# Performance work log

Measured on AMD Instinct MI355X. Metric: run time of the kernel, lower is better.

Reference implementation:

```python
import jax, jax.numpy as jnp
import numpy as np

H, DH, DM = 8, 128, 1024          # n_head, d_head, d_model (n_head*d_head == d_model)
SLEN, BSZ = 256, 64               # slen <= 256 forced by pi0[:, :l]
SCALE = 1.0 / DH ** 0.5
LN_EPS = 1e-5


def setup_inputs() -> dict:
    key = jax.random.key(0)
    k0, k1, k2, k3 = jax.random.split(key, 4)
    h = jax.random.normal(k0, (SLEN, BSZ, DM), jnp.float32)
    W_qkv = jax.random.normal(k1, (H * 4 * DH, DM), jnp.float32) * (DM ** -0.5)
    W_o = jax.random.normal(k2, (DM, H * DH), jnp.float32) * ((H * DH) ** -0.5)
    pi0 = jax.random.uniform(k3, (H, 256), jnp.float32)
    ln_gamma = jnp.ones((DM,), jnp.float32)
    ln_beta = jnp.zeros((DM,), jnp.float32)
    return {"h": h, "W_qkv": W_qkv, "W_o": W_o, "pi0": pi0,
            "ln_gamma": ln_gamma, "ln_beta": ln_beta}


def _phi(x):
    # elu(x)+1 feature map, then L1-normalize over the feature dim
    x = jax.nn.elu(x) + 1.0
    return x / jnp.sum(x, axis=-1, keepdims=True)


def _causal_linear_attn(q, k, v):
    # fast_weight_sum: out_t = sum_{s<=t} (q_t . k_s) v_s  (zero initial fast weights)
    # q,k,v: [b,h,l,d]
    l = q.shape[2]
    scores = jnp.einsum('bhld,bhsd->bhls', q, k)
    mask = jnp.tril(jnp.ones((l, l), dtype=bool))
    scores = jnp.where(mask, scores, jnp.zeros((), scores.dtype))
    return jnp.einsum('bhls,bhsd->bhld', scores, v)


def reference(h, W_qkv, W_o, pi0, ln_gamma, ln_beta):
    l, b, _ = h.shape
    # qkv projection: [l,b,H,4*DH] -> q, k1, k2, v (update_mode='rbf2keys')
    qkv = jnp.einsum('lbm,nm->lbn', h, W_qkv).reshape(l, b, H, 4 * DH)
    q, k1, k2, v = jnp.split(qkv, 4, axis=-1)
    # permute to [b, H, l, d]
    q = _phi(jnp.transpose(q, (1, 2, 0, 3)))
    k1 = _phi(jnp.transpose(k1, (1, 2, 0, 3)))
    k2 = _phi(jnp.transpose(k2, (1, 2, 0, 3)))
    v = jnp.transpose(v, (1, 2, 0, 3))
    # two fast-weight sums (skip_attn_normalization=True path)
    lo1 = _causal_linear_attn(q, k1, v)
    lo2 = _causal_linear_attn(q, k2, v)
    pi = jnp.clip(pi0, 0.0, 1.0)[None, :, :l, None]          # [1,H,l,1]
    layer_out = SCALE * (lo1 * pi + lo2 * (1.0 - pi))         # [b,H,l,d]
    # [b,H,l,d] -> [l,b,H*d]
    layer_out = jnp.transpose(layer_out, (2, 0, 1, 3)).reshape(l, b, H * DH)
    attn_out = jnp.einsum('lbn,mn->lbm', layer_out, W_o)
    # post-LN residual (pre_lnorm=False, dropout=0)
    x = h + attn_out
    mu = jnp.mean(x, axis=-1, keepdims=True)
    var = jnp.mean((x - mu) ** 2, axis=-1, keepdims=True)
    return ln_gamma * (x - mu) / jnp.sqrt(var + LN_EPS) + ln_beta
```

## Files before the change

kernel.cpp:

```cpp
#include <hip/hip_runtime.h>

#define H_     8
#define DM_    1024
#define NQKV_  4096
#define ROWS_  16384
#define PAIRS_ 512
#define SCALE_ 0.08838834764831845f
#define LN_EPS_ 1e-5f

typedef __attribute__((ext_vector_type(8))) short short8;
typedef __attribute__((ext_vector_type(4))) short short4v;
typedef __attribute__((ext_vector_type(4))) float floatx4;

__device__ __forceinline__ float b2f(unsigned short u) {
  union { unsigned int i; float f; } v; v.i = ((unsigned int)u) << 16; return v.f;
}
__device__ __forceinline__ unsigned short f2b(float f) {
  union { unsigned int i; float f; } v; v.f = f;
  unsigned int b = v.i;
  b += 0x7FFFu + ((b >> 16) & 1u);
  return (unsigned short)(b >> 16);
}

__device__ __forceinline__ void gl_lds(const unsigned short* g, unsigned short* s) {
  __builtin_amdgcn_global_load_lds(
      (const __attribute__((address_space(1))) unsigned int*)g,
      (__attribute__((address_space(3))) unsigned int*)s, 16, 0, 0);
}

__device__ __forceinline__ void stage_async(const unsigned short* __restrict__ g,
                                            size_t ld, unsigned short* s, int tid) {
#pragma unroll
  for (int p = 0; p < 4; ++p) {
    int idx = p * 256 + tid;
    int r = idx >> 3, j = idx & 7;
    int cg = j ^ (r & 7);
    gl_lds(g + (size_t)r * ld + cg * 8, s + (size_t)idx * 8);
  }
}
__device__ __forceinline__ void stage_h(const unsigned short* __restrict__ g,
                                        size_t o0, size_t o1,
                                        unsigned short* s, int lo0, int lo1) {
  gl_lds(g + o0, s + lo0);
  gl_lds(g + o1, s + lo1);
}
__device__ __forceinline__ short8 lds_frag(const unsigned short* s, int row, int cg) {
  return *(const short8*)(s + row * 64 + ((cg ^ (row & 7)) << 3));
}

__global__ __launch_bounds__(256) void cvt_all(const float* __restrict__ h,
                                               const float* __restrict__ wq,
                                               const float* __restrict__ wo,
                                               unsigned short* __restrict__ hb,
                                               unsigned short* __restrict__ wqb,
                                               unsigned short* __restrict__ wob) {
  int i = blockIdx.x * 256 + threadIdx.x;
  const float* src; unsigned short* dst; int off;
  if (i < 2097152)      { src = h;  dst = hb;  off = i; }
  else if (i < 2621440) { src = wq; dst = wqb; off = i - 2097152; }
  else                  { src = wo; dst = wob; off = i - 2621440; }
  const float4* s4 = (const float4*)(src + (size_t)off * 8);
  float4 v0 = s4[0], v1 = s4[1];
  union { short8 v; unsigned short u[8]; } pk;
  pk.u[0] = f2b(v0.x); pk.u[1] = f2b(v0.y); pk.u[2] = f2b(v0.z); pk.u[3] = f2b(v0.w);
  pk.u[4] = f2b(v1.x); pk.u[5] = f2b(v1.y); pk.u[6] = f2b(v1.z); pk.u[7] = f2b(v1.w);
  *(short8*)(dst + (size_t)off * 8) = pk.v;
}

__global__ __launch_bounds__(512, 4) void qkv_gemm(const unsigned short* __restrict__ A,
                                                   const unsigned short* __restrict__ B,
                                                   unsigned short* __restrict__ QKV) {
  __shared__ alignas(16) unsigned short Sh[24576];
  unsigned short* As = Sh;
  unsigned short* Bs = Sh + 16384;
  int tid = threadIdx.x;
  int lane = tid & 63, wid = tid >> 6;
  int wm = wid >> 1, wn = wid & 1;
  int quad = lane >> 4, l16 = lane & 15;
  int s7 = l16 & 7;

  int bid = blockIdx.y * 32 + blockIdx.x;
  int swz = (bid & 7) * 256 + (bid >> 3);
  int bx = swz & 31, by = swz >> 5;
  int n0 = bx * 128, hh = bx >> 2, part = bx & 3, bb = by;

  const unsigned short* AbP = A + (size_t)bb * DM_;
  const size_t lda = (size_t)64 * DM_;
  const unsigned short* BbP = B + (size_t)n0 * DM_;

  int r0 = tid >> 3, jj = tid & 7;
  int cg = jj ^ (r0 & 7);
  size_t oA0 = (size_t)r0 * lda + cg * 8;
  size_t oB0 = (size_t)r0 * DM_ + cg * 8;
  int lo = tid * 8;

  floatx4 acc[4][4];
#pragma unroll
  for (int i = 0; i < 4; ++i)
#pragma unroll
    for (int j = 0; j < 4; ++j)
#pragma unroll
      for (int r = 0; r < 4; ++r) acc[i][j][r] = 0.f;

#pragma unroll
  for (int p = 0; p < 4; ++p)
    gl_lds(AbP + oA0 + (size_t)p * 64 * lda, As + lo + p * 4096);
#pragma unroll
  for (int p = 0; p < 2; ++p)
    gl_lds(BbP + oB0 + (size_t)p * 64 * DM_, Bs + lo + p * 4096);

  const unsigned short* aB0 = As + (wm * 64 + l16) * 64 + ((quad ^ s7) << 3);
  const unsigned short* aB1 = As + (wm * 64 + l16) * 64 + (((4 + quad) ^ s7) << 3);
  const unsigned short* bB0 = Bs + (wn * 64 + l16) * 64 + ((quad ^ s7) << 3);
  const unsigned short* bB1 = Bs + (wn * 64 + l16) * 64 + (((4 + quad) ^ s7) << 3);

  for (int t = 0; t < 16; ++t) {
    asm volatile("s_waitcnt vmcnt(0)" ::: "memory");
    __builtin_amdgcn_s_barrier();
    short8 a[4], b[4];
#pragma unroll
    for (int mt = 0; mt < 4; ++mt) a[mt] = *(const short8*)(aB0 + mt * 1024);
#pragma unroll
    for (int nt = 0; nt < 4; ++nt) b[nt] = *(const short8*)(bB0 + nt * 1024);
#pragma unroll
    for (int mt = 0; mt < 4; ++mt)
#pragma unroll
      for (int nt = 0; nt < 4; ++nt)
        acc[mt][nt] = __builtin_amdgcn_mfma_f32_16x16x32_bf16(a[mt], b[nt], acc[mt][nt], 0, 0, 0);
#pragma unroll
    for (int mt = 0; mt < 4; ++mt) a[mt] = *(const short8*)(aB1 + mt * 1024);
#pragma unroll
    for (int nt = 0; nt < 4; ++nt) b[nt] = *(const short8*)(bB1 + nt * 1024);
#pragma unroll
    for (int mt = 0; mt < 4; ++mt)
#pragma unroll
      for (int nt = 0; nt < 4; ++nt)
        acc[mt][nt] = __builtin_amdgcn_mfma_f32_16x16x32_bf16(a[mt], b[nt], acc[mt][nt], 0, 0, 0);
    __syncthreads();
    if (t < 15) {
      size_t kn = (size_t)(t + 1) * 64;
#pragma unroll
      for (int p = 0; p < 4; ++p)
        gl_lds(AbP + kn + oA0 + (size_t)p * 64 * lda, As + lo + p * 4096);
#pragma unroll
      for (int p = 0; p < 2; ++p)
        gl_lds(BbP + kn + oB0 + (size_t)p * 64 * DM_, Bs + lo + p * 4096);
    }
  }

  __syncthreads();
  int c = tid & 15, g = tid >> 4;
  if (part < 3) {
    float rsum[4][4];
#pragma unroll
    for (int mt = 0; mt < 4; ++mt)
#pragma unroll
      for (int r = 0; r < 4; ++r) rsum[mt][r] = 0.f;
#pragma unroll
    for (int mt = 0; mt < 4; ++mt)
#pragma unroll
      for (int nt = 0; nt < 4; ++nt)
#pragma unroll
        for (int r = 0; r < 4; ++r) {
          float x = acc[mt][nt][r];
          float f = x > 0.f ? x + 1.f : __expf(x);
          acc[mt][nt][r] = f;
          rsum[mt][r] += f;
        }
#pragma unroll
    for (int off = 1; off < 16; off <<= 1)
#pragma unroll
      for (int mt = 0; mt < 4; ++mt)
#pragma unroll
        for (int r = 0; r < 4; ++r)
          rsum[mt][r] += __shfl_xor(rsum[mt][r], off);
    float* Pf = (float*)Sh;
    if (l16 == 0) {
#pragma unroll
      for (int mt = 0; mt < 4; ++mt)
#pragma unroll
        for (int r = 0; r < 4; ++r)
          Pf[(wm * 64 + mt * 16 + quad * 4 + r) * 2 + wn] = rsum[mt][r];
    }
    __syncthreads();
    float inv[4][4];
#pragma unroll
    for (int mt = 0; mt < 4; ++mt)
#pragma unroll
      for (int r = 0; r < 4; ++r)
        inv[mt][r] = 1.f / (rsum[mt][r] + Pf[(wm * 64 + mt * 16 + quad * 4 + r) * 2 + (wn ^ 1)]);
    __syncthreads();
    unsigned short* P = QKV + (size_t)part * 16777216 + (size_t)(bb * 8 + hh) * 32768;
#pragma unroll
    for (int hf = 0; hf < 2; ++hf) {
      if ((wm >> 1) == hf) {
#pragma unroll
        for (int mt = 0; mt < 4; ++mt)
#pragma unroll
          for (int nt = 0; nt < 4; ++nt)
#pragma unroll
            for (int r = 0; r < 4; ++r) {
              int row = (wm & 1) * 64 + mt * 16 + quad * 4 + r;
              int col = wn * 64 + nt * 16 + l16;
              Sh[row * 136 + col] = f2b(acc[mt][nt][r] * inv[mt][r]);
            }
      }
      __syncthreads();
#pragma unroll
      for (int j = 0; j < 4; ++j) {
        int row = j * 32 + g;
        *(short8*)(P + (size_t)(hf * 128 + row) * 128 + c * 8) =
            *(const short8*)(Sh + row * 136 + c * 8);
      }
      __syncthreads();
    }
  } else {
    unsigned short* Vt = QKV + (size_t)3 * 16777216 + (size_t)(bb * 8 + hh) * 32768;
#pragma unroll
    for (int hf = 0; hf < 2; ++hf) {
      if ((wm >> 1) == hf) {
#pragma unroll
        for (int mt = 0; mt < 4; ++mt)
#pragma unroll
          for (int nt = 0; nt < 4; ++nt)
#pragma unroll
            for (int r = 0; r < 4; ++r) {
              int d = wn * 64 + nt * 16 + l16;
              int l = (wm & 1) * 64 + mt * 16 + quad * 4 + r;
              Sh[d * 136 + l] = f2b(acc[mt][nt][r]);
            }
      }
      __syncthreads();
#pragma unroll
      for (int j = 0; j < 4; ++j) {
        int d = j * 32 + g;
        *(short8*)(Vt + (size_t)d * 256 + hf * 128 + c * 8) =
            *(const short8*)(Sh + d * 136 + c * 8);
      }
      __syncthreads();
    }
  }
}

#define TILE_BODY(T, BUF, OBUF)                                                \
  {                                                                            \
    unsigned short* SB = (BUF) + 16384;                                        \
    const unsigned short* aA0 = (BUF) + (wm * 128 + l16) * 64 + ((quad ^ s7) << 3); \
    const unsigned short* aA1 = (BUF) + (wm * 128 + l16) * 64 + (((4 + quad) ^ s7) << 3); \
    const unsigned short* bA0 = SB + (wn * 64 + l16) * 64 + ((quad ^ s7) << 3);\
    const unsigned short* bA1 = SB + (wn * 64 + l16) * 64 + (((4 + quad) ^ s7) << 3); \
    short8 a[8], b[4];                                                         \
    if ((T) < 15) {                                                            \
      size_t kn = (size_t)((T) + 1) * 64;                                      \
      stage_h(BbP + kn,  oB0, oB1, (OBUF) + 16384, lo0, lo1);                  \
      stage_h(BbHP + kn, oB0, oB1, (OBUF) + 24576, lo0, lo1);                  \
    }                                                                          \
    _Pragma("unroll")                                                          \
    for (int mt = 0; mt < 4; ++mt) {                                           \
      a[mt * 2 + 0] = *(const short8*)(aA0 + mt * 1024);                       \
      a[mt * 2 + 1] = *(const short8*)(aA1 + mt * 1024);                       \
    }                                                                          \
    _Pragma("unroll")                                                          \
    for (int nt = 0; nt < 2; ++nt) {                                           \
      b[nt * 2 + 0] = *(const short8*)(bA0 + nt * 1024);                       \
      b[nt * 2 + 1] = *(const short8*)(bA1 + nt * 1024);                       \
    }                                                                          \
    __builtin_amdgcn_sched_barrier(0);                                         \
    __builtin_amdgcn_s_barrier();                                              \
    __builtin_amdgcn_s_setprio(1);                                             \
    _Pragma("unroll")                                                          \
    for (int kk = 0; kk < 2; ++kk)                                             \
      _Pragma("unroll")                                                        \
      for (int m = 0; m < 4; ++m)                                              \
        _Pragma("unroll")                                                      \
        for (int n = 0; n < 2; ++n)                                            \
          acc[m][n] = __builtin_amdgcn_mfma_f32_16x16x32_bf16(a[m * 2 + kk], b[n * 2 + kk], acc[m][n], 0, 0, 0); \
    __builtin_amdgcn_s_setprio(0);                                             \
    __builtin_amdgcn_s_barrier();                                              \
    _Pragma("unroll")                                                          \
    for (int nt = 0; nt < 2; ++nt) {                                           \
      b[nt * 2 + 0] = *(const short8*)(bA0 + 2048 + nt * 1024);                \
      b[nt * 2 + 1] = *(const short8*)(bA1 + 2048 + nt * 1024);                \
    }                                                                          \
    __builtin_amdgcn_sched_barrier(0);                                         \
    __builtin_amdgcn_s_barrier();                                              \
    __builtin_amdgcn_s_setprio(1);                                             \
    _Pragma("unroll")                                                          \
    for (int kk = 0; kk < 2; ++kk)                                             \
      _Pragma("unroll")                                                        \
      for (int m = 0; m < 4; ++m)                                              \
        _Pragma("unroll")                                                      \
        for (int n = 0; n < 2; ++n)                                            \
          acc[m][2 + n] = __builtin_amdgcn_mfma_f32_16x16x32_bf16(a[m * 2 + kk], b[n * 2 + kk], acc[m][2 + n], 0, 0, 0); \
    __builtin_amdgcn_s_setprio(0);                                             \
    __builtin_amdgcn_s_barrier();                                              \
    _Pragma("unroll")                                                          \
    for (int mt = 0; mt < 4; ++mt) {                                           \
      a[mt * 2 + 0] = *(const short8*)(aA0 + 4096 + mt * 1024);                \
      a[mt * 2 + 1] = *(const short8*)(aA1 + 4096 + mt * 1024);                \
    }                                                                          \
    __builtin_amdgcn_sched_barrier(0);                                         \
    __builtin_amdgcn_s_barrier();                                              \
    __builtin_amdgcn_s_setprio(1);                                             \
    _Pragma("unroll")                                                          \
    for (int kk = 0; kk < 2; ++kk)                                             \
      _Pragma("unroll")                                                        \
      for (int m = 0; m < 4; ++m)                                              \
        _Pragma("unroll")                                                      \
        for (int n = 0; n < 2; ++n)                                            \
          acc[4 + m][2 + n] = __builtin_amdgcn_mfma_f32_16x16x32_bf16(a[m * 2 + kk], b[n * 2 + kk], acc[4 + m][2 + n], 0, 0, 0); \
    __builtin_amdgcn_s_setprio(0);                                             \
    __builtin_amdgcn_s_barrier();                                              \
    if ((T) < 14) {                                                            \
      size_t kt2 = (size_t)((T) + 2) * 64;                                     \
      stage_h(AbP + kt2,  oA0, oA1, (BUF),        lo0, lo1);                   \
      stage_h(AbHP + kt2, oA0, oA1, (BUF) + 8192, lo0, lo1);                   \
    }                                                                          \
    _Pragma("unroll")                                                          \
    for (int nt = 0; nt < 2; ++nt) {                                           \
      b[nt * 2 + 0] = *(const short8*)(bA0 + nt * 1024);                       \
      b[nt * 2 + 1] = *(const short8*)(bA1 + nt * 1024);                       \
    }                                                                          \
    __builtin_amdgcn_sched_barrier(0);                                         \
    __builtin_amdgcn_s_barrier();                                              \
    __builtin_amdgcn_s_setprio(1);                                             \
    _Pragma("unroll")                                                          \
    for (int kk = 0; kk < 2; ++kk)                                             \
      _Pragma("unroll")                                                        \
      for (int m = 0; m < 4; ++m)                                              \
        _Pragma("unroll")                                                      \
        for (int n = 0; n < 2; ++n)                                            \
          acc[4 + m][n] = __builtin_amdgcn_mfma_f32_16x16x32_bf16(a[m * 2 + kk], b[n * 2 + kk], acc[4 + m][n], 0, 0, 0); \
    __builtin_amdgcn_s_setprio(0);                                             \
    if ((T) < 14) { asm volatile("s_waitcnt vmcnt(4)" ::: "memory"); }         \
    else          { asm volatile("s_waitcnt vmcnt(0)" ::: "memory"); }         \
    __builtin_amdgcn_s_barrier();                                              \
  }

__global__ __launch_bounds__(256) void scores_kernel(const unsigned short* __restrict__ QKV,
                                                     const float* __restrict__ pi0,
                                                     unsigned short* __restrict__ S) {
  __shared__ alignas(16) unsigned short Sh[24576];
  __shared__ float pis[128];
  unsigned short* As  = Sh;
  unsigned short* Bs1 = Sh + 8192;
  unsigned short* Bs2 = Sh + 16384;
  int p = blockIdx.z;
  int hh = p & 7;
  int tid = threadIdx.x;
  int lane = tid & 63, wid = tid >> 6;
  int wm = wid >> 1, wn = wid & 1;
  int quad = lane >> 4, l16 = lane & 15;
  int tix = blockIdx.x;
  int m0 = (tix >= 1) ? 128 : 0;
  int n0 = (tix == 2) ? 128 : 0;
  if (tid < 128) {
    float pv = pi0[hh * 256 + m0 + tid];
    pis[tid] = fminf(fmaxf(pv, 0.f), 1.f);
  }
  const unsigned short* Qb  = QKV + (size_t)p * 32768 + (size_t)m0 * 128;
  const unsigned short* K1b = QKV + 16777216     + (size_t)p * 32768 + (size_t)n0 * 128;
  const unsigned short* K2b = QKV + 2 * 16777216 + (size_t)p * 32768 + (size_t)n0 * 128;

  floatx4 acc1[4][4], acc2[4][4];
#pragma unroll
  for (int i = 0; i < 4; ++i)
#pragma unroll
    for (int j = 0; j < 4; ++j)
#pragma unroll
      for (int r = 0; r < 4; ++r) { acc1[i][j][r] = 0.f; acc2[i][j][r] = 0.f; }

  for (int kt = 0; kt < 128; kt += 64) {
    stage_async(Qb + kt, 128, As, tid);
    stage_async(K1b + kt, 128, Bs1, tid);
    stage_async(K2b + kt, 128, Bs2, tid);
    __syncthreads();
#pragma unroll
    for (int kk = 0; kk < 2; ++kk) {
      short8 af[4], b1[4], b2v[4];
#pragma unroll
      for (int mt = 0; mt < 4; ++mt)
        af[mt] = lds_frag(As, wm * 64 + mt * 16 + l16, kk * 4 + quad);
#pragma unroll
      for (int nt = 0; nt < 4; ++nt) {
        b1[nt]  = lds_frag(Bs1, wn * 64 + nt * 16 + l16, kk * 4 + quad);
        b2v[nt] = lds_frag(Bs2, wn * 64 + nt * 16 + l16, kk * 4 + quad);
      }
#pragma unroll
      for (int mt = 0; mt < 4; ++mt)
#pragma unroll
        for (int nt = 0; nt < 4; ++nt) {
          acc1[mt][nt] = __builtin_amdgcn_mfma_f32_16x16x32_bf16(af[mt], b1[nt],  acc1[mt][nt], 0, 0, 0);
          acc2[mt][nt] = __builtin_amdgcn_mfma_f32_16x16x32_bf16(af[mt], b2v[nt], acc2[mt][nt], 0, 0, 0);
        }
    }
    __syncthreads();
  }
#pragma unroll
  for (int mt = 0; mt < 4; ++mt)
#pragma unroll
    for (int nt = 0; nt < 4; ++nt)
#pragma unroll
      for (int r = 0; r < 4; ++r) {
        int tl = wm * 64 + mt * 16 + quad * 4 + r;
        int sl = wn * 64 + nt * 16 + l16;
        float pv = pis[tl];
        float v = (n0 + sl <= m0 + tl) ? (pv * acc1[mt][nt][r] + (1.f - pv) * acc2[mt][nt][r]) : 0.f;
        Sh[tl * 136 + sl] = f2b(v);
      }
  __syncthreads();
  int c = tid & 15, g = tid >> 4;
#pragma unroll
  for (int j = 0; j < 8; ++j) {
    int r = j * 16 + g;
    size_t gb = (size_t)p * 65536 + (size_t)(m0 + r) * 256 + n0 + c * 8;
    *(short8*)(S + gb) = *(const short8*)(Sh + r * 136 + c * 8);
  }
}

__global__ __launch_bounds__(256, 4) void pv_kernel(const unsigned short* __restrict__ S,
                                                    const unsigned short* __restrict__ Vt,
                                                    unsigned short* __restrict__ LO) {
  __shared__ alignas(16) unsigned short Sh[17408];
  unsigned short* As = Sh;
  unsigned short* Bs = Sh + 8192;
  int p = blockIdx.z;
  int b = p >> 3, hh = p & 7;
  int tid = threadIdx.x;
  int lane = tid & 63, wid = tid >> 6;
  int wm = wid >> 1, wn = wid & 1;
  int quad = lane >> 4, l16 = lane & 15;
  int m0 = blockIdx.y * 128;
  int kEnd = (blockIdx.y == 0) ? 128 : 256;
  const unsigned short* Ab = S  + (size_t)p * 65536 + (size_t)m0 * 256;
  const unsigned short* Bb = Vt + (size_t)p * 32768;

  floatx4 acc[4][4];
#pragma unroll
  for (int i = 0; i < 4; ++i)
#pragma unroll
    for (int j = 0; j < 4; ++j)
#pragma unroll
      for (int r = 0; r < 4; ++r) acc[i][j][r] = 0.f;

  for (int kt = 0; kt < kEnd; kt += 64) {
    stage_async(Ab + kt, 256, As, tid);
    stage_async(Bb + kt, 256, Bs, tid);
    __syncthreads();
#pragma unroll
    for (int kk = 0; kk < 2; ++kk) {
      short8 af[4], bfv[4];
#pragma unroll
      for (int mt = 0; mt < 4; ++mt)
        af[mt] = lds_frag(As, wm * 64 + mt * 16 + l16, kk * 4 + quad);
#pragma unroll
      for (int nt = 0; nt < 4; ++nt)
        bfv[nt] = lds_frag(Bs, wn * 64 + nt * 16 + l16, kk * 4 + quad);
#pragma unroll
      for (int mt = 0; mt < 4; ++mt)
#pragma unroll
        for (int nt = 0; nt < 4; ++nt)
          acc[mt][nt] = __builtin_amdgcn_mfma_f32_16x16x32_bf16(af[mt], bfv[nt], acc[mt][nt], 0, 0, 0);
    }
    __syncthreads();
  }
#pragma unroll
  for (int mt = 0; mt < 4; ++mt)
#pragma unroll
    for (int nt = 0; nt < 4; ++nt)
#pragma unroll
      for (int r = 0; r < 4; ++r) {
        int tl = wm * 64 + mt * 16 + quad * 4 + r;
        int d = wn * 64 + nt * 16 + l16;
        Sh[tl * 136 + d] = f2b(SCALE_ * acc[mt][nt][r]);
      }
  __syncthreads();
  int c = tid & 15, g = tid >> 4;
#pragma unroll
  for (int j = 0; j < 8; ++j) {
    int r = j * 16 + g;
    int t = m0 + r;
    size_t gb = ((size_t)t * 64 + b) * 1024 + hh * 128 + c * 8;
    *(short8*)(LO + gb) = *(const short8*)(Sh + r * 136 + c * 8);
  }
}

__global__ __launch_bounds__(512, 1) void wo_gemm(const unsigned short* __restrict__ A,
                                                  const unsigned short* __restrict__ B,
                                                  unsigned short* __restrict__ attn) {
  __shared__ alignas(16) unsigned short Sh[65536];
  int tid = threadIdx.x;
  int lane = tid & 63, wid = tid >> 6;
  int wm = wid >> 2, wn = wid & 3;
  int quad = lane >> 4, l16 = lane & 15;
  int s7 = l16 & 7;

  int bid = blockIdx.y * 4 + blockIdx.x;
  int swz = (bid & 7) * 32 + (bid >> 3);
  int bx = swz & 3, by = swz >> 2;
  int n0 = bx * 256, m0 = by * 256;

  const unsigned short* AbP = A + (size_t)m0 * DM_;
  const unsigned short* AbHP = AbP + (size_t)128 * DM_;
  const unsigned short* BbP = B + (size_t)n0 * DM_;
  const unsigned short* BbHP = BbP + (size_t)128 * DM_;

  int r0 = tid >> 3, jj = tid & 7;
  int cg = jj ^ (r0 & 7);
  size_t oA0 = (size_t)r0 * DM_ + cg * 8;
  size_t oA1 = (size_t)(r0 + 64) * DM_ + cg * 8;
  size_t oB0 = oA0, oB1 = oA1;
  int lo0 = tid * 8, lo1 = 4096 + tid * 8;

  floatx4 acc[8][4];
#pragma unroll
  for (int i = 0; i < 8; ++i)
#pragma unroll
    for (int j = 0; j < 4; ++j)
#pragma unroll
      for (int r = 0; r < 4; ++r) acc[i][j][r] = 0.f;

  stage_h(AbP,        oA0, oA1, Sh,         lo0, lo1);
  stage_h(AbHP,       oA0, oA1, Sh + 8192,  lo0, lo1);
  stage_h(BbP,        oB0, oB1, Sh + 16384, lo0, lo1);
  stage_h(BbHP,       oB0, oB1, Sh + 24576, lo0, lo1);
  stage_h(AbP + 64,   oA0, oA1, Sh + 32768, lo0, lo1);
  stage_h(AbHP + 64,  oA0, oA1, Sh + 40960, lo0, lo1);
  asm volatile("s_waitcnt vmcnt(4)" ::: "memory");
  __builtin_amdgcn_s_barrier();

  for (int t = 0; t < 16; t += 2) {
    TILE_BODY(t,     Sh,         Sh + 32768)
    TILE_BODY(t + 1, Sh + 32768, Sh)
  }

  __syncthreads();
#pragma unroll
  for (int hq = 0; hq < 2; ++hq) {
    if ((wn >> 1) == hq) {
#pragma unroll
      for (int mt = 0; mt < 8; ++mt)
#pragma unroll
        for (int nt = 0; nt < 4; ++nt)
#pragma unroll
          for (int r = 0; r < 4; ++r) {
            int row = wm * 128 + mt * 16 + quad * 4 + r;
            int col = (wn & 1) * 64 + nt * 16 + l16;
            Sh[row * 136 + col] = f2b(acc[mt][nt][r]);
          }
    }
    __syncthreads();
    int c = tid & 15, g = tid >> 4;
#pragma unroll
    for (int j = 0; j < 8; ++j) {
      int row = j * 32 + g;
      *(short8*)(attn + (size_t)(m0 + row) * DM_ + n0 + hq * 128 + c * 8) =
          *(const short8*)(Sh + row * 136 + c * 8);
    }
    __syncthreads();
  }
}

__global__ __launch_bounds__(256) void ln_res(const unsigned short* __restrict__ attn,
                                              const float* __restrict__ hin,
                                              const float* __restrict__ gamma,
                                              const float* __restrict__ beta,
                                              float* __restrict__ out) {
  int row = blockIdx.x;
  int tid = threadIdx.x;
  const unsigned short* ap = attn + (size_t)row * DM_ + tid * 4;
  const float* hp = hin + (size_t)row * DM_ + tid * 4;
  short4v av = *(const short4v*)ap;
  float4 hv = *(const float4*)hp;
  float x[4];
  x[0] = hv.x + b2f((unsigned short)av[0]);
  x[1] = hv.y + b2f((unsigned short)av[1]);
  x[2] = hv.z + b2f((unsigned short)av[2]);
  x[3] = hv.w + b2f((unsigned short)av[3]);
  float s  = x[0] + x[1] + x[2] + x[3];
  float ss = x[0] * x[0] + x[1] * x[1] + x[2] * x[2] + x[3] * x[3];
#pragma unroll
  for (int off = 32; off; off >>= 1) {
    s  += __shfl_down(s, off);
    ss += __shfl_down(ss, off);
  }
  __shared__ float rs[4], rss[4];
  int wv = tid >> 6, lane = tid & 63;
  if (lane == 0) { rs[wv] = s; rss[wv] = ss; }
  __syncthreads();
  float St  = rs[0] + rs[1] + rs[2] + rs[3];
  float SSt = rss[0] + rss[1] + rss[2] + rss[3];
  float mu = St * (1.f / DM_);
  float var = SSt * (1.f / DM_) - mu * mu;
  float rstd = rsqrtf(var + LN_EPS_);
  float4 o;
#pragma unroll
  for (int j = 0; j < 4; ++j) {
    int c = tid * 4 + j;
    (&o.x)[j] = gamma[c] * (x[j] - mu) * rstd + beta[c];
  }
  *(float4*)(out + (size_t)row * DM_ + tid * 4) = o;
}

extern "C" void kernel_launch(void* const* d_in, const int* in_sizes, int n_in,
                              void* d_out, int out_size, void* d_ws, size_t ws_size,
                              hipStream_t stream) {
  const float* h     = (const float*)d_in[0];
  const float* Wqkv  = (const float*)d_in[1];
  const float* Wo    = (const float*)d_in[2];
  const float* pi0   = (const float*)d_in[3];
  const float* gamma = (const float*)d_in[4];
  const float* beta  = (const float*)d_in[5];
  char* ws = (char*)d_ws;

  unsigned short* QKV   = (unsigned short*)ws;
  unsigned short* Sbuf  = (unsigned short*)(ws + 134217728ull);
  unsigned short* hb    = (unsigned short*)(ws + 134217728ull);
  unsigned short* Wqkvb = (unsigned short*)(ws + 167772160ull);
  unsigned short* Wob   = (unsigned short*)(ws + 201326592ull);
  unsigned short* LO    = (unsigned short*)ws;
  unsigned short* attn  = (unsigned short*)(ws + 134217728ull);
  float* X = (float*)d_out;

  dim3 blk(256);
  cvt_all<<<dim3(10752), blk, 0, stream>>>(h, Wqkv, Wo, hb, Wqkvb, Wob);
  qkv_gemm<<<dim3(32, 64, 1), dim3(512), 0, stream>>>(hb, Wqkvb, QKV);
  scores_kernel<<<dim3(3, 1, PAIRS_), blk, 0, stream>>>(QKV, pi0, Sbuf);
  pv_kernel<<<dim3(1, 2, PAIRS_), blk, 0, stream>>>(Sbuf, QKV + (size_t)3 * 16777216, LO);
  wo_gemm<<<dim3(4, 64, 1), dim3(512), 0, stream>>>(LO, Wob, attn);
  ln_res<<<dim3(ROWS_, 1, 1), blk, 0, stream>>>(attn, h, gamma, beta, X);
}
```

Measured before the change: 498.2 us.

## Enlarge QKV GEMM tile to 256x256 with double-buffered LDS prefetch

The QKV projection GEMM now uses 1024-thread blocks computing 256x256 output tiles (two Q/K/V parts per block) instead of 128x128. The LDS buffer is double-buffered so the next K-slice is prefetched before computing the current one, with a partial vmcnt wait replacing the old wait-all-then-reload pattern. The intent is more operand reuse per load and overlap of global-to-LDS transfers with MFMA work. In exchange, each block uses 128KB of LDS, which limits occupancy to about one block per CU, and the epilogue handling the feature-map normalisation and V transpose is reorganised.

```diff
diff --git a/kernel.cpp b/kernel.cpp
--- a/kernel.cpp
+++ b/kernel.cpp
@@ -67,22 +67,20 @@
   *(short8*)(dst + (size_t)off * 8) = pk.v;
 }
 
-__global__ __launch_bounds__(512, 4) void qkv_gemm(const unsigned short* __restrict__ A,
-                                                   const unsigned short* __restrict__ B,
-                                                   unsigned short* __restrict__ QKV) {
-  __shared__ alignas(16) unsigned short Sh[24576];
-  unsigned short* As = Sh;
-  unsigned short* Bs = Sh + 16384;
+__global__ __launch_bounds__(1024, 4) void qkv_gemm(const unsigned short* __restrict__ A,
+                                                    const unsigned short* __restrict__ B,
+                                                    unsigned short* __restrict__ QKV) {
+  __shared__ alignas(16) unsigned short Sh[65536];
   int tid = threadIdx.x;
   int lane = tid & 63, wid = tid >> 6;
-  int wm = wid >> 1, wn = wid & 1;
+  int wm = wid >> 2, wn = wid & 3;
   int quad = lane >> 4, l16 = lane & 15;
   int s7 = l16 & 7;
 
-  int bid = blockIdx.y * 32 + blockIdx.x;
-  int swz = (bid & 7) * 256 + (bid >> 3);
-  int bx = swz & 31, by = swz >> 5;
-  int n0 = bx * 128, hh = bx >> 2, part = bx & 3, bb = by;
+  int bid = blockIdx.y * 16 + blockIdx.x;
+  int swz = (bid & 7) * 128 + (bid >> 3);
+  int bx = swz & 15, by = swz >> 4;
+  int n0 = bx * 256, hh = bx >> 1, part0 = (bx & 1) * 2, bb = by;
 
   const unsigned short* AbP = A + (size_t)bb * DM_;
   const size_t lda = (size_t)64 * DM_;
@@ -90,8 +88,8 @@
 
   int r0 = tid >> 3, jj = tid & 7;
   int cg = jj ^ (r0 & 7);
-  size_t oA0 = (size_t)r0 * lda + cg * 8;
-  size_t oB0 = (size_t)r0 * DM_ + cg * 8;
+  size_t oA = (size_t)r0 * lda + cg * 8;
+  size_t oB = (size_t)r0 * DM_ + cg * 8;
   int lo = tid * 8;
 
   floatx4 acc[4][4];
@@ -102,21 +100,24 @@
 #pragma unroll
       for (int r = 0; r < 4; ++r) acc[i][j][r] = 0.f;
 
-#pragma unroll
-  for (int p = 0; p < 4; ++p)
-    gl_lds(AbP + oA0 + (size_t)p * 64 * lda, As + lo + p * 4096);
-#pragma unroll
-  for (int p = 0; p < 2; ++p)
-    gl_lds(BbP + oB0 + (size_t)p * 64 * DM_, Bs + lo + p * 4096);
-
-  const unsigned short* aB0 = As + (wm * 64 + l16) * 64 + ((quad ^ s7) << 3);
-  const unsigned short* aB1 = As + (wm * 64 + l16) * 64 + (((4 + quad) ^ s7) << 3);
-  const unsigned short* bB0 = Bs + (wn * 64 + l16) * 64 + ((quad ^ s7) << 3);
-  const unsigned short* bB1 = Bs + (wn * 64 + l16) * 64 + (((4 + quad) ^ s7) << 3);
+#define QSTAGE(KT, SA)                                                         \
+  gl_lds(AbP + (KT) + oA,                     (SA) + lo);                      \
+  gl_lds(AbP + (KT) + oA + (size_t)128 * lda, (SA) + 8192 + lo);               \
+  gl_lds(BbP + (KT) + oB,                     (SA) + 16384 + lo);              \
+  gl_lds(BbP + (KT) + oB + (size_t)128 * DM_, (SA) + 24576 + lo);
+
+  QSTAGE(0, Sh)
 
   for (int t = 0; t < 16; ++t) {
-    asm volatile("s_waitcnt vmcnt(0)" ::: "memory");
+    unsigned short* SA = Sh + (t & 1) * 32768;
+    if (t < 15) { QSTAGE((size_t)(t + 1) * 64, Sh + ((t + 1) & 1) * 32768) }
+    if (t < 15) { asm volatile("s_waitcnt vmcnt(4)" ::: "memory"); }
+    else        { asm volatile("s_waitcnt vmcnt(0)" ::: "memory"); }
     __builtin_amdgcn_s_barrier();
+    const unsigned short* aB0 = SA + (wm * 64 + l16) * 64 + ((quad ^ s7) << 3);
+    const unsigned short* aB1 = SA + (wm * 64 + l16) * 64 + (((4 + quad) ^ s7) << 3);
+    const unsigned short* bB0 = SA + 16384 + (wn * 64 + l16) * 64 + ((quad ^ s7) << 3);
+    const unsigned short* bB1 = SA + 16384 + (wn * 64 + l16) * 64 + (((4 + quad) ^ s7) << 3);
     short8 a[4], b[4];
 #pragma unroll
     for (int mt = 0; mt < 4; ++mt) a[mt] = *(const short8*)(aB0 + mt * 1024);
@@ -136,22 +137,15 @@
 #pragma unroll
       for (int nt = 0; nt < 4; ++nt)
         acc[mt][nt] = __builtin_amdgcn_mfma_f32_16x16x32_bf16(a[mt], b[nt], acc[mt][nt], 0, 0, 0);
-    __syncthreads();
-    if (t < 15) {
-      size_t kn = (size_t)(t + 1) * 64;
-#pragma unroll
-      for (int p = 0; p < 4; ++p)
-        gl_lds(AbP + kn + oA0 + (size_t)p * 64 * lda, As + lo + p * 4096);
-#pragma unroll
-      for (int p = 0; p < 2; ++p)
-        gl_lds(BbP + kn + oB0 + (size_t)p * 64 * DM_, Bs + lo + p * 4096);
-    }
-  }
-
-  __syncthreads();
-  int c = tid & 15, g = tid >> 4;
-  if (part < 3) {
-    float rsum[4][4];
+    __builtin_amdgcn_s_barrier();
+  }
+#undef QSTAGE
+
+  int c16 = tid & 15, g64 = tid >> 4;
+  bool isV = (part0 + (wn >> 1)) == 3;
+  float* Pf = (float*)Sh;
+  float rsum[4][4], inv[4][4];
+  if (!isV) {
 #pragma unroll
     for (int mt = 0; mt < 4; ++mt)
 #pragma unroll
@@ -174,71 +168,70 @@
 #pragma unroll
         for (int r = 0; r < 4; ++r)
           rsum[mt][r] += __shfl_xor(rsum[mt][r], off);
-    float* Pf = (float*)Sh;
     if (l16 == 0) {
 #pragma unroll
       for (int mt = 0; mt < 4; ++mt)
 #pragma unroll
         for (int r = 0; r < 4; ++r)
-          Pf[(wm * 64 + mt * 16 + quad * 4 + r) * 2 + wn] = rsum[mt][r];
+          Pf[(wm * 64 + mt * 16 + quad * 4 + r) * 4 + wn] = rsum[mt][r];
     }
-    __syncthreads();
-    float inv[4][4];
+  }
+  __syncthreads();
+  if (!isV) {
 #pragma unroll
     for (int mt = 0; mt < 4; ++mt)
 #pragma unroll
       for (int r = 0; r < 4; ++r)
-        inv[mt][r] = 1.f / (rsum[mt][r] + Pf[(wm * 64 + mt * 16 + quad * 4 + r) * 2 + (wn ^ 1)]);
-    __syncthreads();
-    unsigned short* P = QKV + (size_t)part * 16777216 + (size_t)(bb * 8 + hh) * 32768;
-#pragma unroll
-    for (int hf = 0; hf < 2; ++hf) {
-      if ((wm >> 1) == hf) {
+        inv[mt][r] = 1.f / (rsum[mt][r] + Pf[(wm * 64 + mt * 16 + quad * 4 + r) * 4 + (wn ^ 1)]);
+  }
+  __syncthreads();
+
+#pragma unroll
+  for (int hq = 0; hq < 2; ++hq) {
+    int part = part0 + hq;
+    if ((wn >> 1) == hq) {
+      if (part < 3) {
 #pragma unroll
         for (int mt = 0; mt < 4; ++mt)
 #pragma unroll
           for (int nt = 0; nt < 4; ++nt)
 #pragma unroll
             for (int r = 0; r < 4; ++r) {
-              int row = (wm & 1) * 64 + mt * 16 + quad * 4 + r;
-              int col = wn * 64 + nt * 16 + l16;
+              int row = wm * 64 + mt * 16 + quad * 4 + r;
+              int col = (wn & 1) * 64 + nt * 16 + l16;
               Sh[row * 136 + col] = f2b(acc[mt][nt][r] * inv[mt][r]);
             }
-      }
-      __syncthreads();
-#pragma unroll
-      for (int j = 0; j < 4; ++j) {
-        int row = j * 32 + g;
-        *(short8*)(P + (size_t)(hf * 128 + row) * 128 + c * 8) =
-            *(const short8*)(Sh + row * 136 + c * 8);
-      }
-      __syncthreads();
-    }
-  } else {
-    unsigned short* Vt = QKV + (size_t)3 * 16777216 + (size_t)(bb * 8 + hh) * 32768;
-#pragma unroll
-    for (int hf = 0; hf < 2; ++hf) {
-      if ((wm >> 1) == hf) {
+      } else {
 #pragma unroll
         for (int mt = 0; mt < 4; ++mt)
 #pragma unroll
           for (int nt = 0; nt < 4; ++nt)
 #pragma unroll
             for (int r = 0; r < 4; ++r) {
-              int d = wn * 64 + nt * 16 + l16;
-              int l = (wm & 1) * 64 + mt * 16 + quad * 4 + r;
-              Sh[d * 136 + l] = f2b(acc[mt][nt][r]);
+              int d = (wn & 1) * 64 + nt * 16 + l16;
+              int l = wm * 64 + mt * 16 + quad * 4 + r;
+              Sh[d * 264 + l] = f2b(acc[mt][nt][r]);
             }
       }
-      __syncthreads();
+    }
+    __syncthreads();
+    if (part < 3) {
+      unsigned short* P = QKV + (size_t)part * 16777216 + (size_t)(bb * 8 + hh) * 32768;
 #pragma unroll
       for (int j = 0; j < 4; ++j) {
-        int d = j * 32 + g;
-        *(short8*)(Vt + (size_t)d * 256 + hf * 128 + c * 8) =
-            *(const short8*)(Sh + d * 136 + c * 8);
+        int row = j * 64 + g64;
+        *(short8*)(P + (size_t)row * 128 + c16 * 8) = *(const short8*)(Sh + row * 136 + c16 * 8);
       }
-      __syncthreads();
+    } else {
+      unsigned short* Vt = QKV + (size_t)3 * 16777216 + (size_t)(bb * 8 + hh) * 32768;
+      int cg2 = tid & 31, g32 = tid >> 5;
+#pragma unroll
+      for (int j = 0; j < 4; ++j) {
+        int d = j * 32 + g32;
+        *(short8*)(Vt + (size_t)d * 256 + cg2 * 8) = *(const short8*)(Sh + d * 264 + cg2 * 8);
+      }
     }
+    __syncthreads();
   }
 }
 
@@ -624,7 +617,7 @@
 
   dim3 blk(256);
   cvt_all<<<dim3(10752), blk, 0, stream>>>(h, Wqkv, Wo, hb, Wqkvb, Wob);
-  qkv_gemm<<<dim3(32, 64, 1), dim3(512), 0, stream>>>(hb, Wqkvb, QKV);
+  qkv_gemm<<<dim3(16, 64, 1), dim3(1024), 0, stream>>>(hb, Wqkvb, QKV);
   scores_kernel<<<dim3(3, 1, PAIRS_), blk, 0, stream>>>(QKV, pi0, Sbuf);
   pv_kernel<<<dim3(1, 2, PAIRS_), blk, 0, stream>>>(Sbuf, QKV + (size_t)3 * 16777216, LO);
   wo_gemm<<<dim3(4, 64, 1), dim3(512), 0, stream>>>(LO, Wob, attn);
```

Result: faster. 419.7 us (-15.8%).
